# Performance work log

Hardware: AMD Instinct MI355X
Metric: run time of the kernel (lower is better)

Reference implementation:

```python
import jax, jax.numpy as jnp
import numpy as np

NUM_HEADS = 12
QK_SCALE = 1.0
EPS = 1e-12  # torch.nn.functional.normalize default eps


def _l2norm(t):
    # matches torch F.normalize: x / max(||x||_2, eps) along last axis
    n = jnp.sqrt(jnp.sum(t * t, axis=-1, keepdims=True))
    return t / jnp.maximum(n, EPS)


def setup_inputs() -> dict:
    key = jax.random.key(0)
    k1, k2 = jax.random.split(key)
    B, N, dim = 8, 4096, 768
    x = jax.random.normal(k1, (B, N, 3 * dim), dtype=jnp.float32)
    temperature = jnp.ones((NUM_HEADS, 1, 1), dtype=jnp.float32)
    proj_w = jax.random.normal(k2, (dim, dim), dtype=jnp.float32) * (1.0 / np.sqrt(dim))
    proj_b = jnp.zeros((dim,), dtype=jnp.float32)
    return {"x": x, "temperature": temperature, "proj_w": proj_w, "proj_b": proj_b}


def reference(x, temperature, proj_w, proj_b):
    B, N, C3 = x.shape
    C = C3 // 3
    H = NUM_HEADS
    d = C // H
    # (B, N, 3, H, d) -> (3, B, H, N, d)
    qkv = x.reshape(B, N, 3, H, d).transpose(2, 0, 3, 1, 4)
    q, k, v = qkv[0], qkv[1], qkv[2]
    q = jnp.swapaxes(q, -2, -1) * QK_SCALE   # [B, H, d, N]
    v = jnp.swapaxes(v, -2, -1)              # [B, H, d, N]
    q = _l2norm(q)                           # normalize over tokens N
    k = _l2norm(k)                           # normalize over head dim d (k is [B,H,N,d])
    # cross-covariance attention over channels: [B, H, d, d]
    attn = jnp.einsum('bhdn,bhne->bhde', q, k) * temperature
    attn = jax.nn.softmax(attn, axis=-1)
    out = jnp.einsum('bhde,bhen->bhdn', attn, v)  # [B, H, d, N]
    out = out.transpose(0, 3, 1, 2).reshape(B, N, C)  # [B, N, C]
    out = out @ proj_w.T + proj_b
    return out
```

## Files before the change

kernel.cpp:

```cpp
#include <hip/hip_runtime.h>
#include <hip/hip_bf16.h>

#define BB 8
#define NN 4096
#define HH 12
#define CC 768
#define C3 2304

typedef float  f32x4  __attribute__((ext_vector_type(4)));
typedef __bf16 bf16x8 __attribute__((ext_vector_type(8)));
typedef __bf16 bf16x4 __attribute__((ext_vector_type(4)));

__device__ __forceinline__ void gload16(const void* g, void* l) {
  __builtin_amdgcn_global_load_lds((const __attribute__((address_space(1))) void*)g,
                                   (__attribute__((address_space(3))) void*)l, 16, 0, 0);
}

__device__ __forceinline__ unsigned int pk2(float a, float b) {
  union { __bf16 h[2]; unsigned int u; } z;
  z.h[0] = (__bf16)a; z.h[1] = (__bf16)b;
  return z.u;
}

__global__ __launch_bounds__(256) void k1_logits(const float* __restrict__ x,
                                                 __bf16* __restrict__ vb,
                                                 float* __restrict__ Spart,
                                                 float* __restrict__ Qpart) {
  const int slice = blockIdx.x;
  const int h = blockIdx.y, b = blockIdx.z;
  const int tid = threadIdx.x;
  __shared__ __bf16 kT[2][64][40];

  const int w = tid >> 6, lane = tid & 63;
  const int fr = lane & 15, fk = lane >> 4;
  const int tp = tid >> 4;
  const int cs = tid & 15;

  const size_t rowbase = (size_t)(b * NN + slice * 256) * C3 + h * 64;
  const float* qp = x + rowbase + w * 16 + fr;
  const float* kp = x + rowbase + 768 + cs * 4;

  const int wblk = ((w ^ (cs & 3)) << 4) + (tp & 3) * 4;
  const int rblk = (fk ^ (fr >> 2)) << 4;

  float qss = 0.f;
  f32x4 acc[4];
#pragma unroll
  for (int tn = 0; tn < 4; ++tn) acc[tn] = (f32x4){0.f, 0.f, 0.f, 0.f};

  bf16x8 afr;
  {
    const int tb = fk * 8;
    const float a0 = qp[(tb + 0) * C3], a1 = qp[(tb + 1) * C3];
    const float a2 = qp[(tb + 2) * C3], a3 = qp[(tb + 3) * C3];
    const float a4 = qp[(tb + 4) * C3], a5 = qp[(tb + 5) * C3];
    const float a6 = qp[(tb + 6) * C3], a7 = qp[(tb + 7) * C3];
    const float4 kv0 = *(const float4*)(kp + (size_t)(2 * tp) * C3);
    const float4 kv1 = *(const float4*)(kp + (size_t)(2 * tp + 1) * C3);
    float s0 = kv0.x * kv0.x + kv0.y * kv0.y + kv0.z * kv0.z + kv0.w * kv0.w;
    float s1 = kv1.x * kv1.x + kv1.y * kv1.y + kv1.z * kv1.z + kv1.w * kv1.w;
    s0 += __shfl_xor(s0, 1); s1 += __shfl_xor(s1, 1);
    s0 += __shfl_xor(s0, 2); s1 += __shfl_xor(s1, 2);
    s0 += __shfl_xor(s0, 4); s1 += __shfl_xor(s1, 4);
    s0 += __shfl_xor(s0, 8); s1 += __shfl_xor(s1, 8);
    const float i0 = 1.0f / fmaxf(sqrtf(s0), 1e-12f);
    const float i1 = 1.0f / fmaxf(sqrtf(s1), 1e-12f);
    char* kbz = (char*)&kT[0][0][0];
    *(unsigned int*)(kbz + (cs * 4 + 0) * 80 + wblk) = pk2(kv0.x * i0, kv1.x * i1);
    *(unsigned int*)(kbz + (cs * 4 + 1) * 80 + wblk) = pk2(kv0.y * i0, kv1.y * i1);
    *(unsigned int*)(kbz + (cs * 4 + 2) * 80 + wblk) = pk2(kv0.z * i0, kv1.z * i1);
    *(unsigned int*)(kbz + (cs * 4 + 3) * 80 + wblk) = pk2(kv0.w * i0, kv1.w * i1);
    qss = a0 * a0 + a1 * a1 + a2 * a2 + a3 * a3 +
          a4 * a4 + a5 * a5 + a6 * a6 + a7 * a7;
    afr[0] = (__bf16)a0; afr[1] = (__bf16)a1; afr[2] = (__bf16)a2; afr[3] = (__bf16)a3;
    afr[4] = (__bf16)a4; afr[5] = (__bf16)a5; afr[6] = (__bf16)a6; afr[7] = (__bf16)a7;
  }
  __syncthreads();

  for (int step = 0; step < 8; ++step) {
    const int cur = step & 1;
    float n0, n1, n2, n3, n4, n5, n6, n7;
    float4 m0, m1;
    if (step < 7) {
      const int tb = (step + 1) * 32 + fk * 8;
      n0 = qp[(tb + 0) * C3]; n1 = qp[(tb + 1) * C3];
      n2 = qp[(tb + 2) * C3]; n3 = qp[(tb + 3) * C3];
      n4 = qp[(tb + 4) * C3]; n5 = qp[(tb + 5) * C3];
      n6 = qp[(tb + 6) * C3]; n7 = qp[(tb + 7) * C3];
      m0 = *(const float4*)(kp + (size_t)((step + 1) * 32 + 2 * tp) * C3);
      m1 = *(const float4*)(kp + (size_t)((step + 1) * 32 + 2 * tp + 1) * C3);
    }
    {
      const char* kbz = (const char*)&kT[cur][0][0];
      const bf16x8 b0 = *(const bf16x8*)(kbz + (0  + fr) * 80 + rblk);
      const bf16x8 b1 = *(const bf16x8*)(kbz + (16 + fr) * 80 + rblk);
      const bf16x8 b2 = *(const bf16x8*)(kbz + (32 + fr) * 80 + rblk);
      const bf16x8 b3 = *(const bf16x8*)(kbz + (48 + fr) * 80 + rblk);
      acc[0] = __builtin_amdgcn_mfma_f32_16x16x32_bf16(afr, b0, acc[0], 0, 0, 0);
      acc[1] = __builtin_amdgcn_mfma_f32_16x16x32_bf16(afr, b1, acc[1], 0, 0, 0);
      acc[2] = __builtin_amdgcn_mfma_f32_16x16x32_bf16(afr, b2, acc[2], 0, 0, 0);
      acc[3] = __builtin_amdgcn_mfma_f32_16x16x32_bf16(afr, b3, acc[3], 0, 0, 0);
    }
    if (step < 7) {
      float s0 = m0.x * m0.x + m0.y * m0.y + m0.z * m0.z + m0.w * m0.w;
      float s1 = m1.x * m1.x + m1.y * m1.y + m1.z * m1.z + m1.w * m1.w;
      s0 += __shfl_xor(s0, 1); s1 += __shfl_xor(s1, 1);
      s0 += __shfl_xor(s0, 2); s1 += __shfl_xor(s1, 2);
      s0 += __shfl_xor(s0, 4); s1 += __shfl_xor(s1, 4);
      s0 += __shfl_xor(s0, 8); s1 += __shfl_xor(s1, 8);
      const float i0 = 1.0f / fmaxf(sqrtf(s0), 1e-12f);
      const float i1 = 1.0f / fmaxf(sqrtf(s1), 1e-12f);
      char* kbz = (char*)&kT[cur ^ 1][0][0];
      *(unsigned int*)(kbz + (cs * 4 + 0) * 80 + wblk) = pk2(m0.x * i0, m1.x * i1);
      *(unsigned int*)(kbz + (cs * 4 + 1) * 80 + wblk) = pk2(m0.y * i0, m1.y * i1);
      *(unsigned int*)(kbz + (cs * 4 + 2) * 80 + wblk) = pk2(m0.z * i0, m1.z * i1);
      *(unsigned int*)(kbz + (cs * 4 + 3) * 80 + wblk) = pk2(m0.w * i0, m1.w * i1);
      qss += n0 * n0 + n1 * n1 + n2 * n2 + n3 * n3 +
             n4 * n4 + n5 * n5 + n6 * n6 + n7 * n7;
      afr[0] = (__bf16)n0; afr[1] = (__bf16)n1; afr[2] = (__bf16)n2; afr[3] = (__bf16)n3;
      afr[4] = (__bf16)n4; afr[5] = (__bf16)n5; afr[6] = (__bf16)n6; afr[7] = (__bf16)n7;
    }
    __syncthreads();
  }

  const int bh = b * HH + h;
  float* Sp = Spart + ((size_t)(slice * 96 + bh)) * 4096;
#pragma unroll
  for (int tn = 0; tn < 4; ++tn)
#pragma unroll
    for (int rr = 0; rr < 4; ++rr)
      Sp[(w * 16 + fk * 4 + rr) * 64 + tn * 16 + fr] = acc[tn][rr];

  {
    float v = qss;
    v += __shfl_xor(v, 16);
    v += __shfl_xor(v, 32);
    if (lane < 16)
      Qpart[((size_t)(slice * 96 + bh)) * 64 + w * 16 + lane] = v;
  }

  const int t = tid >> 3, sub = tid & 7, c0v = sub * 8;
  const float* vsrc = x + (size_t)(b * NN + slice * 256) * C3 + 1536 + h * 64 + c0v;
  __bf16* vdst = vb + (size_t)(b * NN + slice * 256) * CC + h * 64 + c0v;
#pragma unroll
  for (int r = 0; r < 8; ++r) {
    const size_t tok = (size_t)(r * 32 + t);
    const float4 v0 = *(const float4*)(vsrc + tok * C3);
    const float4 v1 = *(const float4*)(vsrc + tok * C3 + 4);
    bf16x8 vv;
    vv[0] = (__bf16)v0.x; vv[1] = (__bf16)v0.y; vv[2] = (__bf16)v0.z; vv[3] = (__bf16)v0.w;
    vv[4] = (__bf16)v1.x; vv[5] = (__bf16)v1.y; vv[6] = (__bf16)v1.z; vv[7] = (__bf16)v1.w;
    *(bf16x8*)(vdst + tok * CC) = vv;
  }
}

__global__ __launch_bounds__(512) void k2_softmax(const float* __restrict__ Spart,
                                                  const float* __restrict__ Qpart,
                                                  const float* __restrict__ temp,
                                                  float* __restrict__ attn) {
  const int h = blockIdx.x, b = blockIdx.y;
  const int tid = threadIdx.x;
  const int i = tid >> 3;
  const int g = tid & 7;
  const int bh = b * HH + h;
  float qs = 0.f;
#pragma unroll
  for (int s = 0; s < 16; ++s) qs += Qpart[((size_t)(s * 96 + bh)) * 64 + i];
  float v[8];
#pragma unroll
  for (int j = 0; j < 8; ++j) v[j] = 0.f;
#pragma unroll 4
  for (int s = 0; s < 16; ++s) {
    const float* Sp = Spart + ((size_t)(s * 96 + bh)) * 4096 + i * 64 + g * 8;
    const float4 t0 = *(const float4*)(Sp);
    const float4 t1 = *(const float4*)(Sp + 4);
    v[0] += t0.x; v[1] += t0.y; v[2] += t0.z; v[3] += t0.w;
    v[4] += t1.x; v[5] += t1.y; v[6] += t1.z; v[7] += t1.w;
  }
  const float rqs = 1.0f / fmaxf(sqrtf(qs), 1e-12f);
  const float tp  = temp[h] * rqs;
  float m = -3.4e38f;
#pragma unroll
  for (int j = 0; j < 8; ++j) { v[j] *= tp; m = fmaxf(m, v[j]); }
  m = fmaxf(m, __shfl_xor(m, 1));
  m = fmaxf(m, __shfl_xor(m, 2));
  m = fmaxf(m, __shfl_xor(m, 4));
  float s = 0.f;
#pragma unroll
  for (int j = 0; j < 8; ++j) { v[j] = __expf(v[j] - m); s += v[j]; }
  s += __shfl_xor(s, 1);
  s += __shfl_xor(s, 2);
  s += __shfl_xor(s, 4);
  const float inv = 1.0f / s;
  float* Ap = attn + (size_t)bh * 4096 + i * 64 + g * 8;
  float4 o0, o1;
  o0.x = v[0] * inv; o0.y = v[1] * inv; o0.z = v[2] * inv; o0.w = v[3] * inv;
  o1.x = v[4] * inv; o1.y = v[5] * inv; o1.z = v[6] * inv; o1.w = v[7] * inv;
  *(float4*)(Ap)     = o0;
  *(float4*)(Ap + 4) = o1;
}

__global__ __launch_bounds__(256) void k3_w2(const float* __restrict__ attn,
                                             const float* __restrict__ pw,
                                             __bf16* __restrict__ W2) {
  const int ct = blockIdx.x, h = blockIdx.y, b = blockIdx.z;
  const int co0 = ct * 64;
  __shared__ float pT[64][65];
  __shared__ float ab[64][64];
  const int tid = threadIdx.x;
  const int r = tid >> 2, c0 = (tid & 3) * 16;
  {
    const float* pp = pw + (size_t)(co0 + r) * CC + h * 64 + c0;
    const float4 p0 = *(const float4*)(pp + 0);
    const float4 p1 = *(const float4*)(pp + 4);
    const float4 p2 = *(const float4*)(pp + 8);
    const float4 p3 = *(const float4*)(pp + 12);
    const float* ap = attn + (size_t)(b * HH + h) * 4096 + r * 64 + c0;
    const float4 a0 = *(const float4*)(ap + 0);
    const float4 a1 = *(const float4*)(ap + 4);
    const float4 a2 = *(const float4*)(ap + 8);
    const float4 a3 = *(const float4*)(ap + 12);
    pT[c0 +  0][r] = p0.x; pT[c0 +  1][r] = p0.y; pT[c0 +  2][r] = p0.z; pT[c0 +  3][r] = p0.w;
    pT[c0 +  4][r] = p1.x; pT[c0 +  5][r] = p1.y; pT[c0 +  6][r] = p1.z; pT[c0 +  7][r] = p1.w;
    pT[c0 +  8][r] = p2.x; pT[c0 +  9][r] = p2.y; pT[c0 + 10][r] = p2.z; pT[c0 + 11][r] = p2.w;
    pT[c0 + 12][r] = p3.x; pT[c0 + 13][r] = p3.y; pT[c0 + 14][r] = p3.z; pT[c0 + 15][r] = p3.w;
    *(float4*)&ab[r][c0 + 0]  = a0;
    *(float4*)&ab[r][c0 + 4]  = a1;
    *(float4*)&ab[r][c0 + 8]  = a2;
    *(float4*)&ab[r][c0 + 12] = a3;
  }
  __syncthreads();
  const int col = tid & 63, jg = tid >> 6;
  float accJ[16];
#pragma unroll
  for (int c = 0; c < 16; ++c) accJ[c] = 0.f;
#pragma unroll 4
  for (int i = 0; i < 64; ++i) {
    const float p = pT[i][col];
    const float4* a4 = (const float4*)&ab[i][jg * 16];
    const float4 A0 = a4[0], A1 = a4[1], A2 = a4[2], A3 = a4[3];
    accJ[0]  = fmaf(p, A0.x, accJ[0]);  accJ[1]  = fmaf(p, A0.y, accJ[1]);
    accJ[2]  = fmaf(p, A0.z, accJ[2]);  accJ[3]  = fmaf(p, A0.w, accJ[3]);
    accJ[4]  = fmaf(p, A1.x, accJ[4]);  accJ[5]  = fmaf(p, A1.y, accJ[5]);
    accJ[6]  = fmaf(p, A1.z, accJ[6]);  accJ[7]  = fmaf(p, A1.w, accJ[7]);
    accJ[8]  = fmaf(p, A2.x, accJ[8]);  accJ[9]  = fmaf(p, A2.y, accJ[9]);
    accJ[10] = fmaf(p, A2.z, accJ[10]); accJ[11] = fmaf(p, A2.w, accJ[11]);
    accJ[12] = fmaf(p, A3.x, accJ[12]); accJ[13] = fmaf(p, A3.y, accJ[13]);
    accJ[14] = fmaf(p, A3.z, accJ[14]); accJ[15] = fmaf(p, A3.w, accJ[15]);
  }
  bf16x8 u0, u1;
#pragma unroll
  for (int c = 0; c < 8; ++c) { u0[c] = (__bf16)accJ[c]; u1[c] = (__bf16)accJ[8 + c]; }
  __bf16* wp = W2 + ((size_t)b * CC + co0 + col) * CC + h * 64 + jg * 16;
  *(bf16x8*)(wp)     = u0;
  *(bf16x8*)(wp + 8) = u1;
}

__global__ __launch_bounds__(256) void k4_gemm(const __bf16* __restrict__ vb,
                                               const __bf16* __restrict__ W2,
                                               const float* __restrict__ pb,
                                               float* __restrict__ out) {
  int id = blockIdx.x;
  const int bz = id / 192;
  const int rem = id - bz * 192;
  const int mg = rem / 48;
  const int idx = rem - mg * 48;
  const int nt = idx >> 3;
  const int mt = mg * 8 + (idx & 7);
  const int m0 = mt * 128, co0 = nt * 128;

  __shared__ __bf16 At[128][32];
  __shared__ __bf16 Bt[128][32];

  const int tid  = threadIdx.x;
  const int w    = tid >> 6, lane = tid & 63;
  const int wm   = w >> 1,   wn   = w & 1;
  const int fr   = lane & 15;
  const int fk   = lane >> 4;

  f32x4 acc[4][4];
#pragma unroll
  for (int tm = 0; tm < 4; ++tm)
#pragma unroll
    for (int tn = 0; tn < 4; ++tn) acc[tm][tn] = (f32x4){0.f, 0.f, 0.f, 0.f};

  const int srow = lane >> 2;
  const int scol = (lane & 3) * 8;
  const __bf16* Ag = vb + (size_t)(bz * NN + m0 + w * 32 + srow) * CC + scol;
  const __bf16* Bg = W2 + ((size_t)bz * CC + co0 + w * 32 + srow) * CC + scol;
  __bf16* lA0 = &At[w * 32][0];
  __bf16* lA1 = &At[w * 32 + 16][0];
  __bf16* lB0 = &Bt[w * 32][0];
  __bf16* lB1 = &Bt[w * 32 + 16][0];

  for (int kk = 0; kk < 24; ++kk) {
    const int kb = kk * 32;
    __syncthreads();
    gload16(Ag + kb,            lA0);
    gload16(Ag + 16 * CC + kb,  lA1);
    gload16(Bg + kb,            lB0);
    gload16(Bg + 16 * CC + kb,  lB1);
    __syncthreads();
    bf16x8 afr[4], bfr[4];
#pragma unroll
    for (int tm = 0; tm < 4; ++tm)
      afr[tm] = *(const bf16x8*)&At[wm * 64 + tm * 16 + fr][fk * 8];
#pragma unroll
    for (int tn = 0; tn < 4; ++tn)
      bfr[tn] = *(const bf16x8*)&Bt[wn * 64 + tn * 16 + fr][fk * 8];
#pragma unroll
    for (int tm = 0; tm < 4; ++tm)
#pragma unroll
      for (int tn = 0; tn < 4; ++tn)
        acc[tm][tn] = __builtin_amdgcn_mfma_f32_16x16x32_bf16(afr[tm], bfr[tn],
                                                              acc[tm][tn], 0, 0, 0);
  }

#pragma unroll
  for (int tn = 0; tn < 4; ++tn) {
    const int co = co0 + wn * 64 + tn * 16 + fr;
    const float bias = pb[co];
#pragma unroll
    for (int tm = 0; tm < 4; ++tm) {
#pragma unroll
      for (int rr = 0; rr < 4; ++rr) {
        const int row = m0 + wm * 64 + tm * 16 + fk * 4 + rr;
        out[(size_t)(bz * NN + row) * CC + co] = acc[tm][tn][rr] + bias;
      }
    }
  }
}

extern "C" void kernel_launch(void* const* d_in, const int* in_sizes, int n_in,
                              void* d_out, int out_size, void* d_ws, size_t ws_size,
                              hipStream_t stream) {
  const float* x    = (const float*)d_in[0];
  const float* temp = (const float*)d_in[1];
  const float* pw   = (const float*)d_in[2];
  const float* pb   = (const float*)d_in[3];
  float* out = (float*)d_out;
  char* ws = (char*)d_ws;

  float*  Spart = (float*)(ws);
  float*  Qpart = (float*)(ws + 25165824);
  float*  attn  = (float*)(ws + 25559040);
  __bf16* W2    = (__bf16*)(ws + 27131904);
  __bf16* vb    = (__bf16*)(ws + 36569088);

  hipLaunchKernelGGL(k1_logits,  dim3(16, 12, 8), dim3(256), 0, stream, x, vb, Spart, Qpart);
  hipLaunchKernelGGL(k2_softmax, dim3(12, 8),     dim3(512), 0, stream, Spart, Qpart, temp, attn);
  hipLaunchKernelGGL(k3_w2,      dim3(12, 12, 8), dim3(256), 0, stream, attn, pw, W2);
  hipLaunchKernelGGL(k4_gemm,    dim3(1536),      dim3(256), 0, stream, vb, W2, pb, out);
}
```

Before: 521.7 us.

## Double-buffer k4 GEMM with BK=64 tiles and XOR-swizzled LDS

Reworks the final projection GEMM to use two LDS buffers with a K-tile of 64, so the global-to-LDS loads for the next tile are issued while MFMAs run on the current one. It also halves the number of barriers per tile and applies an XOR swizzle to the LDS slots to avoid bank conflicts on the fragment reads. The grouped block-to-tile mapping is replaced by a simple row-major one, which may reduce L2 reuse. LDS use doubles, which could lower occupancy.

```diff
diff --git a/kernel.cpp b/kernel.cpp
--- a/kernel.cpp
+++ b/kernel.cpp
@@ -260,72 +260,90 @@
                                                const __bf16* __restrict__ W2,
                                                const float* __restrict__ pb,
                                                float* __restrict__ out) {
-  int id = blockIdx.x;
+  const int id = blockIdx.x;
   const int bz = id / 192;
   const int rem = id - bz * 192;
-  const int mg = rem / 48;
-  const int idx = rem - mg * 48;
-  const int nt = idx >> 3;
-  const int mt = mg * 8 + (idx & 7);
+  const int mt = rem / 6;
+  const int nt = rem - mt * 6;
   const int m0 = mt * 128, co0 = nt * 128;
 
-  __shared__ __bf16 At[128][32];
-  __shared__ __bf16 Bt[128][32];
-
-  const int tid  = threadIdx.x;
-  const int w    = tid >> 6, lane = tid & 63;
-  const int wm   = w >> 1,   wn   = w & 1;
-  const int fr   = lane & 15;
-  const int fk   = lane >> 4;
+  __shared__ __bf16 At[2][128][64];
+  __shared__ __bf16 Bt[2][128][64];
+
+  const int tid = threadIdx.x;
+  const int w = tid >> 6, lane = tid & 63;
+  const int wm = w >> 1, wn = w & 1;
+  const int fr = lane & 15, fk = lane >> 4;
 
   f32x4 acc[4][4];
 #pragma unroll
-  for (int tm = 0; tm < 4; ++tm)
-#pragma unroll
-    for (int tn = 0; tn < 4; ++tn) acc[tm][tn] = (f32x4){0.f, 0.f, 0.f, 0.f};
-
-  const int srow = lane >> 2;
-  const int scol = (lane & 3) * 8;
-  const __bf16* Ag = vb + (size_t)(bz * NN + m0 + w * 32 + srow) * CC + scol;
-  const __bf16* Bg = W2 + ((size_t)bz * CC + co0 + w * 32 + srow) * CC + scol;
-  __bf16* lA0 = &At[w * 32][0];
-  __bf16* lA1 = &At[w * 32 + 16][0];
-  __bf16* lB0 = &Bt[w * 32][0];
-  __bf16* lB1 = &Bt[w * 32 + 16][0];
-
-  for (int kk = 0; kk < 24; ++kk) {
-    const int kb = kk * 32;
+  for (int m = 0; m < 4; ++m)
+#pragma unroll
+    for (int n = 0; n < 4; ++n) acc[m][n] = (f32x4){0.f, 0.f, 0.f, 0.f};
+
+  const int srow  = lane >> 3;
+  const int sslot = (lane & 7) ^ srow;
+  const __bf16* Ag = vb + (size_t)(bz * NN + m0 + w * 8 + srow) * CC + sslot * 8;
+  const __bf16* Bg = W2 + ((size_t)bz * CC + co0 + w * 8 + srow) * CC + sslot * 8;
+
+#define K4_STAGE(buf, kt) do {                                           \
+    const int kb_ = (kt) * 64;                                           \
+    char* la_ = (char*)(&At[buf][0][0]) + w * 1024;                      \
+    char* lb_ = (char*)(&Bt[buf][0][0]) + w * 1024;                      \
+    gload16(Ag + kb_,            la_);                                   \
+    gload16(Ag + 32 * CC + kb_,  la_ + 4096);                            \
+    gload16(Ag + 64 * CC + kb_,  la_ + 8192);                            \
+    gload16(Ag + 96 * CC + kb_,  la_ + 12288);                           \
+    gload16(Bg + kb_,            lb_);                                   \
+    gload16(Bg + 32 * CC + kb_,  lb_ + 4096);                            \
+    gload16(Bg + 64 * CC + kb_,  lb_ + 8192);                            \
+    gload16(Bg + 96 * CC + kb_,  lb_ + 12288);                           \
+  } while (0)
+
+  K4_STAGE(0, 0);
+  __syncthreads();
+
+  const int rsw = fr & 7;
+
+  for (int kt = 0; kt < 12; ++kt) {
+    const int cur = kt & 1;
+    if (kt < 11) K4_STAGE(cur ^ 1, kt + 1);
+
+    const char* Ab = (const char*)&At[cur][0][0];
+    const char* Bb = (const char*)&Bt[cur][0][0];
+    bf16x8 af[2][4], bf[2][4];
+#pragma unroll
+    for (int ks = 0; ks < 2; ++ks) {
+      const int so = ((ks * 4 + fk) ^ rsw) * 16;
+#pragma unroll
+      for (int m = 0; m < 4; ++m)
+        af[ks][m] = *(const bf16x8*)(Ab + (wm * 64 + m * 16 + fr) * 128 + so);
+#pragma unroll
+      for (int n = 0; n < 4; ++n)
+        bf[ks][n] = *(const bf16x8*)(Bb + (wn * 64 + n * 16 + fr) * 128 + so);
+    }
+#pragma unroll
+    for (int ks = 0; ks < 2; ++ks)
+#pragma unroll
+      for (int m = 0; m < 4; ++m)
+#pragma unroll
+        for (int n = 0; n < 4; ++n)
+          acc[m][n] = __builtin_amdgcn_mfma_f32_16x16x32_bf16(af[ks][m], bf[ks][n],
+                                                              acc[m][n], 0, 0, 0);
     __syncthreads();
-    gload16(Ag + kb,            lA0);
-    gload16(Ag + 16 * CC + kb,  lA1);
-    gload16(Bg + kb,            lB0);
-    gload16(Bg + 16 * CC + kb,  lB1);
-    __syncthreads();
-    bf16x8 afr[4], bfr[4];
-#pragma unroll
-    for (int tm = 0; tm < 4; ++tm)
-      afr[tm] = *(const bf16x8*)&At[wm * 64 + tm * 16 + fr][fk * 8];
-#pragma unroll
-    for (int tn = 0; tn < 4; ++tn)
-      bfr[tn] = *(const bf16x8*)&Bt[wn * 64 + tn * 16 + fr][fk * 8];
-#pragma unroll
-    for (int tm = 0; tm < 4; ++tm)
-#pragma unroll
-      for (int tn = 0; tn < 4; ++tn)
-        acc[tm][tn] = __builtin_amdgcn_mfma_f32_16x16x32_bf16(afr[tm], bfr[tn],
-                                                              acc[tm][tn], 0, 0, 0);
-  }
-
-#pragma unroll
-  for (int tn = 0; tn < 4; ++tn) {
-    const int co = co0 + wn * 64 + tn * 16 + fr;
+  }
+#undef K4_STAGE
+
+#pragma unroll
+  for (int n = 0; n < 4; ++n) {
+    const int co = co0 + wn * 64 + n * 16 + fr;
     const float bias = pb[co];
 #pragma unroll
-    for (int tm = 0; tm < 4; ++tm) {
+    for (int m = 0; m < 4; ++m) {
 #pragma unroll
       for (int rr = 0; rr < 4; ++rr) {
-        const int row = m0 + wm * 64 + tm * 16 + fk * 4 + rr;
-        out[(size_t)(bz * NN + row) * CC + co] = acc[tm][tn][rr] + bias;
+        const int row = m0 + wm * 64 + m * 16 + fk * 4 + rr;
+        out[(size_t)(bz * NN + row) * CC + co] = acc[m][n][rr] + bias;
       }
     }
   }
```

Result: slower. 544.3 us (+4.3%).
